# Performance work log

Measured on AMD Instinct MI355X. Metric: run time of the kernel, lower is better.

The kernel has to match this reference:

```python
import jax, jax.numpy as jnp
import numpy as np

LN_EPS = 1e-5


def setup_inputs() -> dict:
    key = jax.random.key(0)
    ks = jax.random.split(key, 8)
    B, S, D = 8, 2048, 1024
    H, A, DA = 16, 4, 64
    sd = 1.0 / np.sqrt(D)
    inp = {
        "x": jax.random.normal(ks[0], (B, S, D), jnp.float32),
        "Wq": jax.random.normal(ks[1], (D, H * DA), jnp.float32) * sd,
        "bq": jnp.zeros((H * DA,), jnp.float32),
        "Wk": jax.random.normal(ks[2], (D, H * DA), jnp.float32) * sd,
        "bk": jnp.zeros((H * DA,), jnp.float32),
        "Wv": jax.random.normal(ks[3], (D, H * DA), jnp.float32) * sd,
        "bv": jnp.zeros((H * DA,), jnp.float32),
        "Wr": jax.random.normal(ks[4], (D, H), jnp.float32) * sd,
        "br": jnp.zeros((H,), jnp.float32),
        "gamma": jnp.ones((H,), jnp.float32),
        "beta": jnp.zeros((H,), jnp.float32),
        "Wo": jax.random.normal(ks[5], (A * DA, D), jnp.float32) * (1.0 / np.sqrt(A * DA)),
        "bo": jnp.zeros((D,), jnp.float32),
        "n_active": 4,
    }
    return inp


def reference(x, Wq, bq, Wk, bk, Wv, bv, Wr, br, gamma, beta, Wo, bo, n_active):
    B, S, D = x.shape
    H = Wr.shape[1]
    DA = Wq.shape[1] // H
    A = int(n_active)

    # --- router (route_type == 'mean', noise == 0) ---
    r = jnp.mean(x @ Wr + br, axis=1)                      # [B, H]
    mu = jnp.mean(r, axis=-1, keepdims=True)
    var = jnp.mean((r - mu) ** 2, axis=-1, keepdims=True)
    rn = (r - mu) * jax.lax.rsqrt(var + LN_EPS) * gamma + beta
    dist = jax.nn.softmax(rn, axis=1)                      # [B, H]

    # top-k heads; boolean-mask gather in torch selects in ascending head order
    _, idx = jax.lax.top_k(dist, A)                        # [B, A]
    idx_sorted = jnp.sort(idx, axis=-1)                    # [B, A]
    dist_dense = jnp.take_along_axis(dist, idx_sorted, axis=-1)  # [B, A]

    def proj(W, b):
        # [B, S, H*DA] -> [B, H, S, DA]
        return (x @ W + b).reshape(B, S, H, DA).transpose(0, 2, 1, 3)

    gidx = idx_sorted[:, :, None, None]                    # [B, A, 1, 1]
    Q = jnp.take_along_axis(proj(Wq, bq), gidx, axis=1)    # [B, A, S, DA]
    K = jnp.take_along_axis(proj(Wk, bk), gidx, axis=1)
    V = jnp.take_along_axis(proj(Wv, bv), gidx, axis=1)

    scale = 1.0 / jnp.sqrt(jnp.asarray(DA, x.dtype))
    scores = jnp.einsum("basd,batd->bast", Q, K) * scale   # [B, A, S, S]
    attn = jax.nn.softmax(scores, axis=-1)
    O = jnp.einsum("bast,batd->basd", attn, V)             # [B, A, S, DA]

    O = dist_dense[:, :, None, None] * O                   # gated combine
    O_final = O.transpose(0, 2, 1, 3).reshape(B, S, A * DA)
    Z = O_final @ Wo + bo                                  # [B, S, D]
    return Z
```

## Files before the change

kernel.cpp:

```cpp
#include <hip/hip_runtime.h>
#include <math.h>

#define B_ 8
#define S_ 2048
#define D_ 1024
#define H_ 16
#define A_ 4
#define DA_ 64
#define LN_EPS 1e-5f
#define QSCALE 0.1803368801111204f
#define MREF 20.0f

typedef __bf16 bf16x8 __attribute__((ext_vector_type(8)));
typedef __bf16 bf16x4 __attribute__((ext_vector_type(4)));
typedef float f32x4 __attribute__((ext_vector_type(4)));
typedef unsigned short u16x8 __attribute__((ext_vector_type(8)));

static const size_t OFF_PARTIAL = 0;
static const size_t OFF_LPART   = 0;
static const size_t OFF_IDX     = (size_t)1 << 20;
static const size_t OFF_DIST    = ((size_t)1 << 20) + 1024;
static const size_t OFF_WOT     = ((size_t)1 << 20) + ((size_t)1 << 19);
static const size_t OFF_XB      = (size_t)2 << 20;
static const size_t OFF_OPART   = OFF_XB;
static const size_t OFF_WT      = (size_t)34 << 20;
static const size_t OFF_Q       = (size_t)40 << 20;
static const size_t OFF_OFIN    = OFF_Q;
static const size_t OFF_K       = (size_t)48 << 20;
static const size_t OFF_V       = (size_t)56 << 20;

__global__ __launch_bounds__(256) void k_partial(const float* __restrict__ x,
                                                 float* __restrict__ partial,
                                                 __bf16* __restrict__ xb) {
  const int c = blockIdx.x, b = blockIdx.y, t = threadIdx.x;
  const size_t base = ((size_t)b * S_ + (size_t)c * 64) * D_;
  f32x4 acc = {0.f, 0.f, 0.f, 0.f};
  for (int s = 0; s < 64; ++s) {
    f32x4 v = *(const f32x4*)(x + base + (size_t)s * D_ + 4 * t);
    acc += v;
    bf16x4 o;
    #pragma unroll
    for (int j = 0; j < 4; ++j) o[j] = (__bf16)v[j];
    *(bf16x4*)(xb + base + (size_t)s * D_ + 4 * t) = o;
  }
  *(f32x4*)(partial + ((size_t)b * 32 + c) * D_ + 4 * t) = acc;
}

__global__ __launch_bounds__(256) void k_wt(const float* __restrict__ Wq,
                                            const float* __restrict__ Wk,
                                            const float* __restrict__ Wv,
                                            __bf16* __restrict__ Wt) {
  __shared__ float tsh[64][65];
  const int n0 = blockIdx.x * 64, k0 = blockIdx.y * 64, z = blockIdx.z;
  const float* W = (z == 0) ? Wq : (z == 1) ? Wk : Wv;
  const int t = threadIdx.x;
  #pragma unroll
  for (int i = 0; i < 4; ++i) {
    int r = i * 16 + (t >> 4), c = (t & 15) * 4;
    f32x4 v = *(const f32x4*)(W + (size_t)(k0 + r) * (H_ * DA_) + n0 + c);
    tsh[r][c + 0] = v[0]; tsh[r][c + 1] = v[1]; tsh[r][c + 2] = v[2]; tsh[r][c + 3] = v[3];
  }
  __syncthreads();
  #pragma unroll
  for (int i = 0; i < 4; ++i) {
    int n = i * 16 + (t >> 4), kc = (t & 15) * 4;
    bf16x4 o;
    #pragma unroll
    for (int j = 0; j < 4; ++j) o[j] = (__bf16)tsh[kc + j][n];
    *(bf16x4*)(Wt + (size_t)z * 1048576 + (size_t)(n0 + n) * 1024 + k0 + kc) = o;
  }
}

__global__ __launch_bounds__(256) void k_wto(const float* __restrict__ Wo,
                                             __bf16* __restrict__ WoT) {
  __shared__ float tsh[64][65];
  const int n0 = blockIdx.x * 64, k0 = blockIdx.y * 64;
  const int t = threadIdx.x;
  #pragma unroll
  for (int i = 0; i < 4; ++i) {
    int r = i * 16 + (t >> 4), c = (t & 15) * 4;
    f32x4 v = *(const f32x4*)(Wo + (size_t)(k0 + r) * D_ + n0 + c);
    tsh[r][c + 0] = v[0]; tsh[r][c + 1] = v[1]; tsh[r][c + 2] = v[2]; tsh[r][c + 3] = v[3];
  }
  __syncthreads();
  #pragma unroll
  for (int i = 0; i < 4; ++i) {
    int n = i * 16 + (t >> 4), kc = (t & 15) * 4;
    bf16x4 o;
    #pragma unroll
    for (int j = 0; j < 4; ++j) o[j] = (__bf16)tsh[kc + j][n];
    *(bf16x4*)(WoT + (size_t)(n0 + n) * (A_ * DA_) + k0 + kc) = o;
  }
}

__global__ __launch_bounds__(256) void k_stats(const float* __restrict__ partial,
                                               const float* __restrict__ Wr,
                                               const float* __restrict__ br,
                                               const float* __restrict__ gamma,
                                               const float* __restrict__ beta,
                                               int* __restrict__ idx_out,
                                               float* __restrict__ dist_out) {
  __shared__ float xbar[D_];
  __shared__ float rsh[H_];
  const int b = blockIdx.x, t = threadIdx.x;
  #pragma unroll
  for (int j = 0; j < 4; ++j) {
    int d = j * 256 + t;
    float s = 0.f;
    for (int c = 0; c < 32; ++c) s += partial[((size_t)b * 32 + c) * D_ + d];
    xbar[d] = s * (1.0f / S_);
  }
  __syncthreads();
  const int w = t >> 6, lane = t & 63;
  #pragma unroll
  for (int i = 0; i < 4; ++i) {
    int h = w * 4 + i;
    float s = 0.f;
    #pragma unroll
    for (int j = 0; j < 16; ++j) {
      int d = j * 64 + lane;
      s += xbar[d] * Wr[d * H_ + h];
    }
    for (int off = 32; off; off >>= 1) s += __shfl_down(s, off);
    if (lane == 0) rsh[h] = s + br[h];
  }
  __syncthreads();
  if (t == 0) {
    float r[H_];
    float mu = 0.f;
    for (int h = 0; h < H_; ++h) { r[h] = rsh[h]; mu += r[h]; }
    mu *= (1.0f / H_);
    float var = 0.f;
    for (int h = 0; h < H_; ++h) { float d = r[h] - mu; var += d * d; }
    var *= (1.0f / H_);
    float inv = rsqrtf(var + LN_EPS);
    float rn[H_], ex[H_];
    float mx = -1e30f;
    for (int h = 0; h < H_; ++h) {
      rn[h] = (r[h] - mu) * inv * gamma[h] + beta[h];
      mx = fmaxf(mx, rn[h]);
    }
    float sum = 0.f;
    for (int h = 0; h < H_; ++h) { ex[h] = expf(rn[h] - mx); sum += ex[h]; }
    int sel[A_];
    bool used[H_] = {false};
    for (int a = 0; a < A_; ++a) {
      int best = 0; float bv = -1.f;
      for (int h = 0; h < H_; ++h)
        if (!used[h] && ex[h] > bv) { bv = ex[h]; best = h; }
      used[best] = true; sel[a] = best;
    }
    for (int i = 0; i < A_; ++i)
      for (int j = i + 1; j < A_; ++j)
        if (sel[j] < sel[i]) { int tmp = sel[i]; sel[i] = sel[j]; sel[j] = tmp; }
    float invsum = 1.0f / sum;
    for (int a = 0; a < A_; ++a) {
      idx_out[b * A_ + a] = sel[a];
      dist_out[b * A_ + a] = ex[sel[a]] * invsum;
    }
  }
}

__global__ __launch_bounds__(256) void k_qkv_mfma(const __bf16* __restrict__ xb,
                                                  const __bf16* __restrict__ Wt,
                                                  const float* __restrict__ bq,
                                                  const float* __restrict__ bk,
                                                  const float* __restrict__ bv,
                                                  const int* __restrict__ idx,
                                                  __bf16* __restrict__ Q,
                                                  __bf16* __restrict__ K,
                                                  __bf16* __restrict__ Vt_g) {
  __shared__ unsigned short As[64][72];
  __shared__ unsigned short Bs[192][72];
  const int qt = blockIdx.x, ba = blockIdx.y;
  const int b = ba >> 2;
  const int head64 = idx[ba] * 64;
  const int t = threadIdx.x;
  const int w = t >> 6, l = t & 63, x = l & 15, g = l >> 4;
  const int MO = (w >> 1) * 32, NO = (w & 1) * 96;

  const unsigned short* xbu = (const unsigned short*)xb;
  const unsigned short* Wtu = (const unsigned short*)Wt;
  const size_t xbase = ((size_t)b * S_ + (size_t)qt * 64) * D_;

  u16x8 areg[2], breg[6];
  #pragma unroll
  for (int i = 0; i < 2; ++i) {
    int id = t + 256 * i, row = id >> 3, ch = id & 7;
    areg[i] = *(const u16x8*)(xbu + xbase + (size_t)row * D_ + ch * 8);
  }
  #pragma unroll
  for (int i = 0; i < 6; ++i) {
    int id = t + 256 * i, row = id >> 3, ch = id & 7;
    int m = row >> 6, nn = row & 63;
    breg[i] = *(const u16x8*)(Wtu + (size_t)m * 1048576 +
                              (size_t)(head64 + nn) * 1024 + ch * 8);
  }

  f32x4 acc[2][6];
  #pragma unroll
  for (int mf = 0; mf < 2; ++mf)
    #pragma unroll
    for (int nf = 0; nf < 6; ++nf) acc[mf][nf] = (f32x4){0.f, 0.f, 0.f, 0.f};

  for (int k0 = 0; k0 < D_; k0 += 64) {
    __syncthreads();
    #pragma unroll
    for (int i = 0; i < 2; ++i) {
      int id = t + 256 * i, row = id >> 3, ch = id & 7;
      *(u16x8*)&As[row][ch * 8] = areg[i];
    }
    #pragma unroll
    for (int i = 0; i < 6; ++i) {
      int id = t + 256 * i, row = id >> 3, ch = id & 7;
      *(u16x8*)&Bs[row][ch * 8] = breg[i];
    }
    __syncthreads();
    {
      int kn = (k0 + 64 < D_) ? k0 + 64 : k0;
      #pragma unroll
      for (int i = 0; i < 2; ++i) {
        int id = t + 256 * i, row = id >> 3, ch = id & 7;
        areg[i] = *(const u16x8*)(xbu + xbase + (size_t)row * D_ + kn + ch * 8);
      }
      #pragma unroll
      for (int i = 0; i < 6; ++i) {
        int id = t + 256 * i, row = id >> 3, ch = id & 7;
        int m = row >> 6, nn = row & 63;
        breg[i] = *(const u16x8*)(Wtu + (size_t)m * 1048576 +
                                  (size_t)(head64 + nn) * 1024 + kn + ch * 8);
      }
    }
    #pragma unroll
    for (int ks = 0; ks < 2; ++ks) {
      bf16x8 af[2], bfr[6];
      #pragma unroll
      for (int mf = 0; mf < 2; ++mf)
        af[mf] = *(const bf16x8*)&As[MO + mf * 16 + x][ks * 32 + g * 8];
      #pragma unroll
      for (int nf = 0; nf < 6; ++nf)
        bfr[nf] = *(const bf16x8*)&Bs[NO + nf * 16 + x][ks * 32 + g * 8];
      #pragma unroll
      for (int mf = 0; mf < 2; ++mf)
        #pragma unroll
        for (int nf = 0; nf < 6; ++nf)
          acc[mf][nf] = __builtin_amdgcn_mfma_f32_16x16x32_bf16(af[mf], bfr[nf], acc[mf][nf], 0, 0, 0);
    }
  }

  #pragma unroll
  for (int nf = 0; nf < 6; ++nf) {
    const int n = NO + nf * 16;
    const int m = n >> 6;
    if (m == 2) continue;
    const float* bias = (m == 0) ? bq : bk;
    __bf16* out = (m == 0) ? Q : K;
    const float sc = (m == 0) ? QSCALE : 1.0f;
    const int nn = (n & 63) + x;
    const float bval = bias[head64 + nn];
    #pragma unroll
    for (int mf = 0; mf < 2; ++mf)
      #pragma unroll
      for (int r = 0; r < 4; ++r) {
        int srow = qt * 64 + MO + mf * 16 + 4 * g + r;
        float val = (acc[mf][nf][r] + bval) * sc;
        out[((size_t)ba * S_ + srow) * DA_ + nn] = (__bf16)val;
      }
  }

  __syncthreads();
  if (w & 1) {
    #pragma unroll
    for (int nf = 2; nf < 6; ++nf) {
      const int da = (nf - 2) * 16 + x;
      const float bval = bv[head64 + da];
      #pragma unroll
      for (int mf = 0; mf < 2; ++mf)
        #pragma unroll
        for (int r = 0; r < 4; ++r) {
          int ls = MO + mf * 16 + 4 * g + r;
          __bf16 vb = (__bf16)(acc[mf][nf][r] + bval);
          As[da][ls] = __builtin_bit_cast(unsigned short, vb);
        }
    }
  }
  __syncthreads();
  {
    unsigned short* Vtu = (unsigned short*)Vt_g;
    const int vrow = t >> 3, vch = t & 7;
    u16x8 v0 = *(const u16x8*)&As[vrow][vch * 8];
    u16x8 v1 = *(const u16x8*)&As[vrow + 32][vch * 8];
    const size_t vb0 = (size_t)ba * DA_ * S_;
    *(u16x8*)(Vtu + vb0 + (size_t)vrow * S_ + qt * 64 + vch * 8) = v0;
    *(u16x8*)(Vtu + vb0 + (size_t)(vrow + 32) * S_ + qt * 64 + vch * 8) = v1;
  }
}

__global__ __launch_bounds__(256, 4) void k_attn_mfma(const __bf16* __restrict__ Qg,
                                                      const __bf16* __restrict__ Kg,
                                                      const __bf16* __restrict__ Vtg,
                                                      float* __restrict__ Opart,
                                                      float* __restrict__ lpart) {
  __shared__ unsigned short QPs[64 * 72];
  __shared__ unsigned short Ks[64 * 64];
  __shared__ unsigned short Vt[64 * 64];

  const int qt = blockIdx.x, ba = blockIdx.y, z = blockIdx.z;
  const int t = threadIdx.x;
  const int w = t >> 6, l = t & 63, x = l & 15, g = l >> 4;

  const unsigned short* Qgu = (const unsigned short*)Qg;
  const unsigned short* Kgu = (const unsigned short*)Kg;
  const unsigned short* Vgu = (const unsigned short*)Vtg;

  const size_t kvbase = (size_t)ba * S_ * DA_;
  const size_t vbase  = (size_t)ba * DA_ * S_;
  const int klo = z * 16, khi = klo + 16;

  const int krow = t >> 3, kch = t & 7;

  u16x8 kreg0, kreg1, vreg0, vreg1;
  kreg0 = *(const u16x8*)(Kgu + kvbase + (size_t)(klo * 64 + krow) * 64 + kch * 8);
  kreg1 = *(const u16x8*)(Kgu + kvbase + (size_t)(klo * 64 + krow + 32) * 64 + kch * 8);
  vreg0 = *(const u16x8*)(Vgu + vbase + (size_t)krow * S_ + klo * 64 + kch * 8);
  vreg1 = *(const u16x8*)(Vgu + vbase + (size_t)(krow + 32) * S_ + klo * 64 + kch * 8);

  {
    const size_t qbase = ((size_t)ba * S_ + (size_t)qt * 64) * DA_;
    #pragma unroll
    for (int i = 0; i < 2; ++i) {
      int row = (t >> 3) + 32 * i;
      int ch = t & 7;
      u16x8 v = *(const u16x8*)(Qgu + qbase + (size_t)row * 64 + ch * 8);
      *(u16x8*)&QPs[row * 64 + ((ch ^ (row & 7)) << 3)] = v;
    }
  }
  __syncthreads();

  bf16x8 qf[2];
  #pragma unroll
  for (int ks = 0; ks < 2; ++ks) {
    int row = w * 16 + x;
    int ch = (g + 4 * ks) ^ (row & 7);
    qf[ks] = *(const bf16x8*)&QPs[row * 64 + (ch << 3)];
  }

  f32x4 o_[4];
  float l_[4];
  #pragma unroll
  for (int r = 0; r < 4; ++r) l_[r] = 0.f;
  #pragma unroll
  for (int nf = 0; nf < 4; ++nf) o_[nf] = (f32x4){0.f, 0.f, 0.f, 0.f};

  for (int kt = klo; kt < khi; ++kt) {
    __syncthreads();
    *(u16x8*)&Ks[krow * 64 + ((kch ^ (krow & 7)) << 3)] = kreg0;
    *(u16x8*)&Vt[krow * 64 + ((kch ^ (krow & 7)) << 3)] = vreg0;
    {
      int row1 = krow + 32;
      *(u16x8*)&Ks[row1 * 64 + ((kch ^ (row1 & 7)) << 3)] = kreg1;
      *(u16x8*)&Vt[row1 * 64 + ((kch ^ (row1 & 7)) << 3)] = vreg1;
    }
    __syncthreads();

    {
      int ktn = (kt + 1 < khi) ? kt + 1 : kt;
      kreg0 = *(const u16x8*)(Kgu + kvbase + (size_t)(ktn * 64 + krow) * 64 + kch * 8);
      kreg1 = *(const u16x8*)(Kgu + kvbase + (size_t)(ktn * 64 + krow + 32) * 64 + kch * 8);
      vreg0 = *(const u16x8*)(Vgu + vbase + (size_t)krow * S_ + ktn * 64 + kch * 8);
      vreg1 = *(const u16x8*)(Vgu + vbase + (size_t)(krow + 32) * S_ + ktn * 64 + kch * 8);
    }

    f32x4 s_[4];
    #pragma unroll
    for (int nf = 0; nf < 4; ++nf) s_[nf] = (f32x4){-MREF, -MREF, -MREF, -MREF};
    #pragma unroll
    for (int ks = 0; ks < 2; ++ks) {
      bf16x8 kf[4];
      #pragma unroll
      for (int nf = 0; nf < 4; ++nf) {
        int kvrow = nf * 16 + x;
        int ch = (g + 4 * ks) ^ (kvrow & 7);
        kf[nf] = *(const bf16x8*)&Ks[kvrow * 64 + (ch << 3)];
      }
      #pragma unroll
      for (int nf = 0; nf < 4; ++nf)
        s_[nf] = __builtin_amdgcn_mfma_f32_16x16x32_bf16(qf[ks], kf[nf], s_[nf], 0, 0, 0);
    }

    #pragma unroll
    for (int r = 0; r < 4; ++r) {
      float rs = 0.f;
      #pragma unroll
      for (int nf = 0; nf < 4; ++nf) {
        float p = exp2f(s_[nf][r]);
        s_[nf][r] = p;
        rs += p;
      }
      l_[r] += rs;
    }

    #pragma unroll
    for (int nf = 0; nf < 4; ++nf)
      #pragma unroll
      for (int r = 0; r < 4; ++r) {
        int row = w * 16 + 4 * g + r;
        int col = nf * 16 + x;
        __bf16 pb = (__bf16)s_[nf][r];
        QPs[row * 72 + col] = __builtin_bit_cast(unsigned short, pb);
      }

    #pragma unroll
    for (int ks = 0; ks < 2; ++ks) {
      bf16x8 pf = *(const bf16x8*)&QPs[(w * 16 + x) * 72 + (g * 8 + ks * 32)];
      bf16x8 vf[4];
      #pragma unroll
      for (int nf = 0; nf < 4; ++nf) {
        int darow = nf * 16 + x;
        int ch = (g + 4 * ks) ^ (darow & 7);
        vf[nf] = *(const bf16x8*)&Vt[darow * 64 + (ch << 3)];
      }
      #pragma unroll
      for (int nf = 0; nf < 4; ++nf)
        o_[nf] = __builtin_amdgcn_mfma_f32_16x16x32_bf16(pf, vf[nf], o_[nf], 0, 0, 0);
    }
  }

  float* Op = Opart + (size_t)z * ((size_t)B_ * A_ * S_ * DA_);
  #pragma unroll
  for (int r = 0; r < 4; ++r) {
    float lr = l_[r];
    lr += __shfl_xor(lr, 1);
    lr += __shfl_xor(lr, 2);
    lr += __shfl_xor(lr, 4);
    lr += __shfl_xor(lr, 8);
    if (x == 0) {
      int row = qt * 64 + w * 16 + 4 * g + r;
      lpart[(size_t)z * (B_ * A_ * S_) + (size_t)ba * S_ + row] = lr;
    }
  }
  #pragma unroll
  for (int nf = 0; nf < 4; ++nf)
    #pragma unroll
    for (int r = 0; r < 4; ++r) {
      int row = qt * 64 + w * 16 + 4 * g + r;
      int col = nf * 16 + x;
      Op[((size_t)ba * S_ + row) * DA_ + col] = o_[nf][r];
    }
}

__global__ __launch_bounds__(256) void k_combine(const float* __restrict__ Opart,
                                                 const float* __restrict__ lpart,
                                                 const float* __restrict__ dist,
                                                 __bf16* __restrict__ Ofin) {
  const size_t e = ((size_t)blockIdx.x * 256 + threadIdx.x) * 8;
  const int row = (int)(e >> 6);
  const int col = (int)(e & 63);
  const int ba = row >> 11, s = row & (S_ - 1);
  const int b = ba >> 2, a = ba & 3;
  const float* Op1 = Opart + (size_t)B_ * A_ * S_ * DA_;
  f32x4 p00 = *(const f32x4*)(Opart + (size_t)row * DA_ + col);
  f32x4 p01 = *(const f32x4*)(Opart + (size_t)row * DA_ + col + 4);
  f32x4 p10 = *(const f32x4*)(Op1 + (size_t)row * DA_ + col);
  f32x4 p11 = *(const f32x4*)(Op1 + (size_t)row * DA_ + col + 4);
  const float ls = lpart[row] + lpart[B_ * A_ * S_ + row];
  const float sc = dist[ba] / ls;
  bf16x8 o;
  #pragma unroll
  for (int j = 0; j < 4; ++j) o[j] = (__bf16)((p00[j] + p10[j]) * sc);
  #pragma unroll
  for (int j = 0; j < 4; ++j) o[4 + j] = (__bf16)((p01[j] + p11[j]) * sc);
  *(bf16x8*)(Ofin + ((size_t)(b * S_ + s)) * (A_ * DA_) + a * DA_ + col) = o;
}

__global__ __launch_bounds__(256) void k_oproj_mfma(const __bf16* __restrict__ Of,
                                                    const __bf16* __restrict__ WoT,
                                                    const float* __restrict__ bo,
                                                    float* __restrict__ Z) {
  __shared__ unsigned short As[128][72];
  __shared__ unsigned short Bs[128][72];
  const int nt = blockIdx.x, mt = blockIdx.y;
  const int t = threadIdx.x;
  const int w = t >> 6, l = t & 63, x = l & 15, g = l >> 4;
  const int MO = (w >> 1) * 64, NO = (w & 1) * 64;

  const unsigned short* Ofu = (const unsigned short*)Of;
  const unsigned short* Wu  = (const unsigned short*)WoT;

  f32x4 acc[4][4];
  #pragma unroll
  for (int mf = 0; mf < 4; ++mf)
    #pragma unroll
    for (int nf = 0; nf < 4; ++nf) acc[mf][nf] = (f32x4){0.f, 0.f, 0.f, 0.f};

  for (int k0 = 0; k0 < A_ * DA_; k0 += 64) {
    #pragma unroll
    for (int i = 0; i < 4; ++i) {
      int id = t + 256 * i;
      int row = id >> 3, ch = id & 7;
      u16x8 v = *(const u16x8*)(Ofu + ((size_t)(mt * 128 + row)) * (A_ * DA_) + k0 + ch * 8);
      *(u16x8*)&As[row][ch * 8] = v;
    }
    #pragma unroll
    for (int i = 0; i < 4; ++i) {
      int id = t + 256 * i;
      int row = id >> 3, ch = id & 7;
      u16x8 v = *(const u16x8*)(Wu + ((size_t)(nt * 128 + row)) * (A_ * DA_) + k0 + ch * 8);
      *(u16x8*)&Bs[row][ch * 8] = v;
    }
    __syncthreads();
    #pragma unroll
    for (int ks = 0; ks < 2; ++ks) {
      bf16x8 af[4], bfr[4];
      #pragma unroll
      for (int mf = 0; mf < 4; ++mf)
        af[mf] = *(const bf16x8*)&As[MO + mf * 16 + x][ks * 32 + g * 8];
      #pragma unroll
      for (int nf = 0; nf < 4; ++nf)
        bfr[nf] = *(const bf16x8*)&Bs[NO + nf * 16 + x][ks * 32 + g * 8];
      #pragma unroll
      for (int mf = 0; mf < 4; ++mf)
        #pragma unroll
        for (int nf = 0; nf < 4; ++nf)
          acc[mf][nf] = __builtin_amdgcn_mfma_f32_16x16x32_bf16(af[mf], bfr[nf], acc[mf][nf], 0, 0, 0);
    }
    __syncthreads();
  }

  #pragma unroll
  for (int nf = 0; nf < 4; ++nf) {
    const int n = nt * 128 + NO + nf * 16 + x;
    const float bval = bo[n];
    #pragma unroll
    for (int mf = 0; mf < 4; ++mf)
      #pragma unroll
      for (int r = 0; r < 4; ++r) {
        int row = mt * 128 + MO + mf * 16 + 4 * g + r;
        Z[(size_t)row * D_ + n] = acc[mf][nf][r] + bval;
      }
  }
}

extern "C" void kernel_launch(void* const* d_in, const int* in_sizes, int n_in,
                              void* d_out, int out_size, void* d_ws, size_t ws_size,
                              hipStream_t stream) {
  const float* x     = (const float*)d_in[0];
  const float* Wq    = (const float*)d_in[1];
  const float* bq    = (const float*)d_in[2];
  const float* Wk    = (const float*)d_in[3];
  const float* bk    = (const float*)d_in[4];
  const float* Wv    = (const float*)d_in[5];
  const float* bv    = (const float*)d_in[6];
  const float* Wr    = (const float*)d_in[7];
  const float* br    = (const float*)d_in[8];
  const float* gamma = (const float*)d_in[9];
  const float* beta  = (const float*)d_in[10];
  const float* Wo    = (const float*)d_in[11];
  const float* bo    = (const float*)d_in[12];
  float* Z = (float*)d_out;

  char* ws = (char*)d_ws;
  float*  partial = (float*)(ws + OFF_PARTIAL);
  float*  lpart   = (float*)(ws + OFF_LPART);
  int*    idx     = (int*)(ws + OFF_IDX);
  float*  dist    = (float*)(ws + OFF_DIST);
  __bf16* WoT     = (__bf16*)(ws + OFF_WOT);
  __bf16* xb      = (__bf16*)(ws + OFF_XB);
  float*  Opart   = (float*)(ws + OFF_OPART);
  __bf16* Wt      = (__bf16*)(ws + OFF_WT);
  __bf16* Q       = (__bf16*)(ws + OFF_Q);
  __bf16* Ofin    = (__bf16*)(ws + OFF_OFIN);
  __bf16* K       = (__bf16*)(ws + OFF_K);
  __bf16* Vt      = (__bf16*)(ws + OFF_V);

  k_partial<<<dim3(32, B_), 256, 0, stream>>>(x, partial, xb);
  k_wt<<<dim3(16, 16, 3), 256, 0, stream>>>(Wq, Wk, Wv, Wt);
  k_wto<<<dim3(16, 4), 256, 0, stream>>>(Wo, WoT);
  k_stats<<<B_, 256, 0, stream>>>(partial, Wr, br, gamma, beta, idx, dist);
  k_qkv_mfma<<<dim3(S_ / 64, B_ * A_), 256, 0, stream>>>(xb, Wt, bq, bk, bv, idx, Q, K, Vt);
  k_attn_mfma<<<dim3(S_ / 64, B_ * A_, 2), 256, 0, stream>>>(Q, K, Vt, Opart, lpart);
  k_combine<<<2048, 256, 0, stream>>>(Opart, lpart, dist, Ofin);
  k_oproj_mfma<<<dim3(D_ / 128, (B_ * S_) / 128), 256, 0, stream>>>(Ofin, WoT, bo, Z);
}
```

Before: 191.9 us.

## Drop split-KV in attention, fuse combine epilogue, prefetch oproj tiles

The attention kernel no longer splits the key range across two z-blocks. Each block now walks all 32 KV tiles and writes the normalized, gate-scaled bf16 output directly, which removes the k_combine kernel and its fp32 partial round-trip through memory. The grid shrinks from 2048 to 1024 blocks, so occupancy and parallelism on the GPU drop. The output-projection GEMM now register-prefetches the next K tile while computing the current one, and moves its barrier accordingly.

```diff
diff --git a/kernel.cpp b/kernel.cpp
--- a/kernel.cpp
+++ b/kernel.cpp
@@ -17,15 +17,13 @@
 typedef unsigned short u16x8 __attribute__((ext_vector_type(8)));
 
 static const size_t OFF_PARTIAL = 0;
-static const size_t OFF_LPART   = 0;
 static const size_t OFF_IDX     = (size_t)1 << 20;
 static const size_t OFF_DIST    = ((size_t)1 << 20) + 1024;
 static const size_t OFF_WOT     = ((size_t)1 << 20) + ((size_t)1 << 19);
 static const size_t OFF_XB      = (size_t)2 << 20;
-static const size_t OFF_OPART   = OFF_XB;
+static const size_t OFF_OFIN    = OFF_XB;
 static const size_t OFF_WT      = (size_t)34 << 20;
 static const size_t OFF_Q       = (size_t)40 << 20;
-static const size_t OFF_OFIN    = OFF_Q;
 static const size_t OFF_K       = (size_t)48 << 20;
 static const size_t OFF_V       = (size_t)56 << 20;
 
@@ -299,13 +297,14 @@
 __global__ __launch_bounds__(256, 4) void k_attn_mfma(const __bf16* __restrict__ Qg,
                                                       const __bf16* __restrict__ Kg,
                                                       const __bf16* __restrict__ Vtg,
-                                                      float* __restrict__ Opart,
-                                                      float* __restrict__ lpart) {
+                                                      const float* __restrict__ dist,
+                                                      __bf16* __restrict__ Ofin) {
   __shared__ unsigned short QPs[64 * 72];
   __shared__ unsigned short Ks[64 * 64];
   __shared__ unsigned short Vt[64 * 64];
 
-  const int qt = blockIdx.x, ba = blockIdx.y, z = blockIdx.z;
+  const int qt = blockIdx.x, ba = blockIdx.y;
+  const int b = ba >> 2, a = ba & 3;
   const int t = threadIdx.x;
   const int w = t >> 6, l = t & 63, x = l & 15, g = l >> 4;
 
@@ -315,15 +314,14 @@
 
   const size_t kvbase = (size_t)ba * S_ * DA_;
   const size_t vbase  = (size_t)ba * DA_ * S_;
-  const int klo = z * 16, khi = klo + 16;
 
   const int krow = t >> 3, kch = t & 7;
 
   u16x8 kreg0, kreg1, vreg0, vreg1;
-  kreg0 = *(const u16x8*)(Kgu + kvbase + (size_t)(klo * 64 + krow) * 64 + kch * 8);
-  kreg1 = *(const u16x8*)(Kgu + kvbase + (size_t)(klo * 64 + krow + 32) * 64 + kch * 8);
-  vreg0 = *(const u16x8*)(Vgu + vbase + (size_t)krow * S_ + klo * 64 + kch * 8);
-  vreg1 = *(const u16x8*)(Vgu + vbase + (size_t)(krow + 32) * S_ + klo * 64 + kch * 8);
+  kreg0 = *(const u16x8*)(Kgu + kvbase + (size_t)(krow) * 64 + kch * 8);
+  kreg1 = *(const u16x8*)(Kgu + kvbase + (size_t)(krow + 32) * 64 + kch * 8);
+  vreg0 = *(const u16x8*)(Vgu + vbase + (size_t)krow * S_ + kch * 8);
+  vreg1 = *(const u16x8*)(Vgu + vbase + (size_t)(krow + 32) * S_ + kch * 8);
 
   {
     const size_t qbase = ((size_t)ba * S_ + (size_t)qt * 64) * DA_;
@@ -352,7 +350,7 @@
   #pragma unroll
   for (int nf = 0; nf < 4; ++nf) o_[nf] = (f32x4){0.f, 0.f, 0.f, 0.f};
 
-  for (int kt = klo; kt < khi; ++kt) {
+  for (int kt = 0; kt < 32; ++kt) {
     __syncthreads();
     *(u16x8*)&Ks[krow * 64 + ((kch ^ (krow & 7)) << 3)] = kreg0;
     *(u16x8*)&Vt[krow * 64 + ((kch ^ (krow & 7)) << 3)] = vreg0;
@@ -364,7 +362,7 @@
     __syncthreads();
 
     {
-      int ktn = (kt + 1 < khi) ? kt + 1 : kt;
+      int ktn = (kt + 1 < 32) ? kt + 1 : kt;
       kreg0 = *(const u16x8*)(Kgu + kvbase + (size_t)(ktn * 64 + krow) * 64 + kch * 8);
       kreg1 = *(const u16x8*)(Kgu + kvbase + (size_t)(ktn * 64 + krow + 32) * 64 + kch * 8);
       vreg0 = *(const u16x8*)(Vgu + vbase + (size_t)krow * S_ + ktn * 64 + kch * 8);
@@ -426,51 +424,28 @@
     }
   }
 
-  float* Op = Opart + (size_t)z * ((size_t)B_ * A_ * S_ * DA_);
-  #pragma unroll
-  for (int r = 0; r < 4; ++r) {
-    float lr = l_[r];
-    lr += __shfl_xor(lr, 1);
-    lr += __shfl_xor(lr, 2);
-    lr += __shfl_xor(lr, 4);
-    lr += __shfl_xor(lr, 8);
-    if (x == 0) {
-      int row = qt * 64 + w * 16 + 4 * g + r;
-      lpart[(size_t)z * (B_ * A_ * S_) + (size_t)ba * S_ + row] = lr;
-    }
-  }
-  #pragma unroll
-  for (int nf = 0; nf < 4; ++nf)
+  const float dd = dist[ba];
+  {
+    float inv[4];
     #pragma unroll
     for (int r = 0; r < 4; ++r) {
-      int row = qt * 64 + w * 16 + 4 * g + r;
-      int col = nf * 16 + x;
-      Op[((size_t)ba * S_ + row) * DA_ + col] = o_[nf][r];
-    }
-}
-
-__global__ __launch_bounds__(256) void k_combine(const float* __restrict__ Opart,
-                                                 const float* __restrict__ lpart,
-                                                 const float* __restrict__ dist,
-                                                 __bf16* __restrict__ Ofin) {
-  const size_t e = ((size_t)blockIdx.x * 256 + threadIdx.x) * 8;
-  const int row = (int)(e >> 6);
-  const int col = (int)(e & 63);
-  const int ba = row >> 11, s = row & (S_ - 1);
-  const int b = ba >> 2, a = ba & 3;
-  const float* Op1 = Opart + (size_t)B_ * A_ * S_ * DA_;
-  f32x4 p00 = *(const f32x4*)(Opart + (size_t)row * DA_ + col);
-  f32x4 p01 = *(const f32x4*)(Opart + (size_t)row * DA_ + col + 4);
-  f32x4 p10 = *(const f32x4*)(Op1 + (size_t)row * DA_ + col);
-  f32x4 p11 = *(const f32x4*)(Op1 + (size_t)row * DA_ + col + 4);
-  const float ls = lpart[row] + lpart[B_ * A_ * S_ + row];
-  const float sc = dist[ba] / ls;
-  bf16x8 o;
-  #pragma unroll
-  for (int j = 0; j < 4; ++j) o[j] = (__bf16)((p00[j] + p10[j]) * sc);
-  #pragma unroll
-  for (int j = 0; j < 4; ++j) o[4 + j] = (__bf16)((p01[j] + p11[j]) * sc);
-  *(bf16x8*)(Ofin + ((size_t)(b * S_ + s)) * (A_ * DA_) + a * DA_ + col) = o;
+      float lr = l_[r];
+      lr += __shfl_xor(lr, 1);
+      lr += __shfl_xor(lr, 2);
+      lr += __shfl_xor(lr, 4);
+      lr += __shfl_xor(lr, 8);
+      inv[r] = dd / lr;
+    }
+    #pragma unroll
+    for (int nf = 0; nf < 4; ++nf)
+      #pragma unroll
+      for (int r = 0; r < 4; ++r) {
+        int row = qt * 64 + w * 16 + 4 * g + r;
+        int col = nf * 16 + x;
+        Ofin[((size_t)b * S_ + row) * (A_ * DA_) + a * DA_ + col] =
+            (__bf16)(o_[nf][r] * inv[r]);
+      }
+  }
 }
 
 __global__ __launch_bounds__(256) void k_oproj_mfma(const __bf16* __restrict__ Of,
@@ -487,6 +462,14 @@
   const unsigned short* Ofu = (const unsigned short*)Of;
   const unsigned short* Wu  = (const unsigned short*)WoT;
 
+  u16x8 areg[4], breg[4];
+  #pragma unroll
+  for (int i = 0; i < 4; ++i) {
+    int id = t + 256 * i, row = id >> 3, ch = id & 7;
+    areg[i] = *(const u16x8*)(Ofu + ((size_t)(mt * 128 + row)) * (A_ * DA_) + ch * 8);
+    breg[i] = *(const u16x8*)(Wu + ((size_t)(nt * 128 + row)) * (A_ * DA_) + ch * 8);
+  }
+
   f32x4 acc[4][4];
   #pragma unroll
   for (int mf = 0; mf < 4; ++mf)
@@ -494,21 +477,23 @@
     for (int nf = 0; nf < 4; ++nf) acc[mf][nf] = (f32x4){0.f, 0.f, 0.f, 0.f};
 
   for (int k0 = 0; k0 < A_ * DA_; k0 += 64) {
+    __syncthreads();
     #pragma unroll
     for (int i = 0; i < 4; ++i) {
-      int id = t + 256 * i;
-      int row = id >> 3, ch = id & 7;
-      u16x8 v = *(const u16x8*)(Ofu + ((size_t)(mt * 128 + row)) * (A_ * DA_) + k0 + ch * 8);
-      *(u16x8*)&As[row][ch * 8] = v;
-    }
-    #pragma unroll
-    for (int i = 0; i < 4; ++i) {
-      int id = t + 256 * i;
-      int row = id >> 3, ch = id & 7;
-      u16x8 v = *(const u16x8*)(Wu + ((size_t)(nt * 128 + row)) * (A_ * DA_) + k0 + ch * 8);
-      *(u16x8*)&Bs[row][ch * 8] = v;
+      int id = t + 256 * i, row = id >> 3, ch = id & 7;
+      *(u16x8*)&As[row][ch * 8] = areg[i];
+      *(u16x8*)&Bs[row][ch * 8] = breg[i];
     }
     __syncthreads();
+    {
+      int kn = (k0 + 64 < A_ * DA_) ? k0 + 64 : k0;
+      #pragma unroll
+      for (int i = 0; i < 4; ++i) {
+        int id = t + 256 * i, row = id >> 3, ch = id & 7;
+        areg[i] = *(const u16x8*)(Ofu + ((size_t)(mt * 128 + row)) * (A_ * DA_) + kn + ch * 8);
+        breg[i] = *(const u16x8*)(Wu + ((size_t)(nt * 128 + row)) * (A_ * DA_) + kn + ch * 8);
+      }
+    }
     #pragma unroll
     for (int ks = 0; ks < 2; ++ks) {
       bf16x8 af[4], bfr[4];
@@ -524,7 +509,6 @@
         for (int nf = 0; nf < 4; ++nf)
           acc[mf][nf] = __builtin_amdgcn_mfma_f32_16x16x32_bf16(af[mf], bfr[nf], acc[mf][nf], 0, 0, 0);
     }
-    __syncthreads();
   }
 
   #pragma unroll
@@ -561,12 +545,10 @@
 
   char* ws = (char*)d_ws;
   float*  partial = (float*)(ws + OFF_PARTIAL);
-  float*  lpart   = (float*)(ws + OFF_LPART);
   int*    idx     = (int*)(ws + OFF_IDX);
   float*  dist    = (float*)(ws + OFF_DIST);
   __bf16* WoT     = (__bf16*)(ws + OFF_WOT);
   __bf16* xb      = (__bf16*)(ws + OFF_XB);
-  float*  Opart   = (float*)(ws + OFF_OPART);
   __bf16* Wt      = (__bf16*)(ws + OFF_WT);
   __bf16* Q       = (__bf16*)(ws + OFF_Q);
   __bf16* Ofin    = (__bf16*)(ws + OFF_OFIN);
@@ -578,7 +560,6 @@
   k_wto<<<dim3(16, 4), 256, 0, stream>>>(Wo, WoT);
   k_stats<<<B_, 256, 0, stream>>>(partial, Wr, br, gamma, beta, idx, dist);
   k_qkv_mfma<<<dim3(S_ / 64, B_ * A_), 256, 0, stream>>>(xb, Wt, bq, bk, bv, idx, Q, K, Vt);
-  k_attn_mfma<<<dim3(S_ / 64, B_ * A_, 2), 256, 0, stream>>>(Q, K, Vt, Opart, lpart);
-  k_combine<<<2048, 256, 0, stream>>>(Opart, lpart, dist, Ofin);
+  k_attn_mfma<<<dim3(S_ / 64, B_ * A_), 256, 0, stream>>>(Q, K, Vt, dist, Ofin);
   k_oproj_mfma<<<dim3(D_ / 128, (B_ * S_) / 128), 256, 0, stream>>>(Ofin, WoT, bo, Z);
 }
```

Measured after the change: 176.5 us. 1.09x faster.
